# Kernel optimization log

Hardware: AMD Instinct MI355X
Metric: run time of the kernel (lower is better)

The kernel has to match this reference:

```python
import jax, jax.numpy as jnp
import numpy as np

HIDDEN = 512
REL = 16
N = 256
BSZ = 32


def setup_inputs() -> dict:
    key = jax.random.key(0)
    ks = jax.random.split(key, 8)
    columns = jax.random.normal(ks[0], (BSZ, N, HIDDEN), dtype=jnp.float32)
    logits = jax.random.normal(ks[1], (BSZ, N, 2), dtype=jnp.float32)
    adj = jax.random.randint(ks[2], (BSZ, N, N), 0, REL)
    # proj: Linear(2+hidden, hidden); stored as [in, out] so x @ W_proj + b_proj
    W_proj = jax.random.normal(ks[3], (2 + HIDDEN, HIDDEN), dtype=jnp.float32) / np.sqrt(2 + HIDDEN)
    b_proj = jnp.zeros((HIDDEN,), dtype=jnp.float32)
    ln_g = jnp.ones((HIDDEN,), dtype=jnp.float32)
    ln_b = jnp.zeros((HIDDEN,), dtype=jnp.float32)
    # low-rank relation weights: W [h,3,h], V [R,3] (xavier-ish)
    W = jax.random.normal(ks[4], (HIDDEN, 3, HIDDEN), dtype=jnp.float32) * np.sqrt(2.0 / (HIDDEN + HIDDEN))
    V = jax.random.normal(ks[5], (REL, 3), dtype=jnp.float32) * np.sqrt(2.0 / (REL + 3))
    return {"columns": columns, "logits": logits, "adj": adj,
            "W_proj": W_proj, "b_proj": b_proj, "ln_g": ln_g, "ln_b": ln_b,
            "W": W, "V": V}


def reference(columns, logits, adj, W_proj, b_proj, ln_g, ln_b, W, V):
    # proj + layernorm + gelu (dropout is identity in deterministic reference)
    h = jnp.concatenate([columns, logits], axis=-1) @ W_proj + b_proj  # [b,n,h]
    mu = jnp.mean(h, axis=-1, keepdims=True)
    var = jnp.mean(jnp.square(h - mu), axis=-1, keepdims=True)
    h = (h - mu) * jax.lax.rsqrt(var + 1e-5) * ln_g + ln_b
    x = jax.nn.gelu(h, approximate=False)  # torch nn.GELU default = exact erf

    R = V.shape[0]
    # low-rank relation weight mixing: Wr[r] = sum_t V[r,t] * W[:,t,:] -> [R,h,h]
    Wr = jnp.einsum('rt,hto->rho', V, W)

    # relation 0 uses identity adjacency (support = x); relations 1..R-1 use adj==r masks
    masks = (adj[..., None] == jnp.arange(1, R)).astype(x.dtype)  # [b,n,n,R-1]
    sup = jnp.einsum('bnmr,bmh->brnh', masks, x)                  # [b,R-1,n,h]

    out = jnp.einsum('bnh,ho->bno', x, Wr[0]) + jnp.einsum('brnh,rho->bno', sup, Wr[1:])
    return out
```

## Files before the change

### kernel.cpp

```cpp
#include <hip/hip_runtime.h>
#include <math.h>

#define HID 512
#define NSEQ 256
#define BSZ 32
#define ROWS (BSZ*NSEQ)
#define KP 576

typedef _Float16 half8_t __attribute__((ext_vector_type(8)));
typedef _Float16 half4_t __attribute__((ext_vector_type(4)));
typedef float f32x4 __attribute__((ext_vector_type(4)));

__device__ __forceinline__ void gload16(const _Float16* g, _Float16* l) {
    __builtin_amdgcn_global_load_lds(
        (const __attribute__((address_space(1))) unsigned int*)g,
        (__attribute__((address_space(3))) unsigned int*)l, 16, 0, 0);
}

__global__ __launch_bounds__(256) void prep(
    const float* __restrict__ cols, const float* __restrict__ logits,
    const float* __restrict__ Wp, const float* __restrict__ W,
    const int* __restrict__ adj, const float* __restrict__ V,
    _Float16* __restrict__ Acat, _Float16* __restrict__ WpT,
    _Float16* __restrict__ WcT, _Float16* __restrict__ C16b)
{
    __shared__ _Float16 ts[64][68];
    __shared__ _Float16 lutH[48];
    __shared__ _Float16 V0h[3];
    const int blk = blockIdx.x, tid = threadIdx.x;

    if (blk < 1024) {
        int row0 = blk * 8;
        #pragma unroll
        for (int rr = 0; rr < 8; ++rr) {
            int row = row0 + rr;
            for (int k = tid; k < KP; k += 256) {
                float v = 0.f;
                if (k < 512) v = cols[(size_t)row*512 + k];
                else if (k < 514) v = logits[(size_t)row*2 + (k-512)];
                Acat[(size_t)row*KP + k] = (_Float16)v;
            }
        }
    } else if (blk < 1216) {
        int sub = blk - 1024;
        int c0 = (sub % 24) * 64, h0 = (sub / 24) * 64;
        int r = tid >> 2, q = tid & 3;
        #pragma unroll
        for (int i = 0; i < 4; ++i) {
            float4 v = *(const float4*)&W[(size_t)(h0+r)*1536 + c0 + q*16 + i*4];
            ts[r][q*16+i*4+0] = (_Float16)v.x;
            ts[r][q*16+i*4+1] = (_Float16)v.y;
            ts[r][q*16+i*4+2] = (_Float16)v.z;
            ts[r][q*16+i*4+3] = (_Float16)v.w;
        }
        __syncthreads();
        _Float16* op = WcT + (size_t)(c0 + r)*512 + h0 + q*16;
        #pragma unroll
        for (int i = 0; i < 4; ++i) {
            half4_t o;
            #pragma unroll
            for (int j = 0; j < 4; ++j) o[j] = ts[q*16+i*4+j][r];
            *(half4_t*)(op + i*4) = o;
        }
    } else if (blk < 1288) {
        int sub = blk - 1216;
        int k0 = (sub % 9) * 64, o0 = (sub / 9) * 64;
        int r = tid >> 2, q = tid & 3;
        int k = k0 + r;
        #pragma unroll
        for (int i = 0; i < 4; ++i) {
            float4 v = make_float4(0.f,0.f,0.f,0.f);
            if (k < 514) v = *(const float4*)&Wp[(size_t)k*HID + o0 + q*16 + i*4];
            ts[r][q*16+i*4+0] = (_Float16)v.x;
            ts[r][q*16+i*4+1] = (_Float16)v.y;
            ts[r][q*16+i*4+2] = (_Float16)v.z;
            ts[r][q*16+i*4+3] = (_Float16)v.w;
        }
        __syncthreads();
        _Float16* op = WpT + (size_t)(o0 + r)*KP + k0 + q*16;
        #pragma unroll
        for (int i = 0; i < 4; ++i) {
            half4_t o;
            #pragma unroll
            for (int j = 0; j < 4; ++j) o[j] = ts[q*16+i*4+j][r];
            *(half4_t*)(op + i*4) = o;
        }
    } else {
        if (tid < 48) { int r = tid/3; lutH[tid] = (_Float16)((r >= 1) ? V[tid] : 0.f); }
        if (tid < 3) V0h[tid] = (_Float16)V[tid];
        __syncthreads();
        int sub = blk - 1288;
        int b = sub >> 2, nt = sub & 3;
        int w = tid >> 6, lane = tid & 63;
        #pragma unroll
        for (int i = 0; i < 16; ++i) {
            int n = nt*64 + w*16 + i;
            int4 a4 = *(const int4*)(adj + ((size_t)(b*NSEQ + n))*NSEQ + lane*4);
            int av[4] = { a4.x, a4.y, a4.z, a4.w };
            size_t ob = ((size_t)(b*NSEQ + n))*768 + lane*4;
            #pragma unroll
            for (int t = 0; t < 3; ++t) {
                half4_t o;
                #pragma unroll
                for (int j = 0; j < 4; ++j) o[j] = lutH[av[j]*3 + t];
                if ((n >> 2) == lane) o[n & 3] = (_Float16)(o[n & 3] + V0h[t]);
                *(half4_t*)(C16b + ob + (size_t)t*256) = o;
            }
        }
    }
}

template<int KS, int NKT, int DEPTH, int NB, int NBLK, int EPI>
__global__ __launch_bounds__(512) void gemm512(
    const _Float16* __restrict__ A, const _Float16* __restrict__ Bm,
    const float* __restrict__ bias, void* __restrict__ outv)
{
    __shared__ _Float16 smem[DEPTH * 2 * 8192];
    _Float16* As = smem;
    _Float16* Bs = smem + DEPTH * 8192;
    const int tid = threadIdx.x;
    const int w = tid >> 6, lane = tid & 63;
    const int ell = blockIdx.x;
    const int s = (ell & 7) * (NB / 8) + (ell >> 3);
    const int row0 = (s / NBLK) * 128, col0 = (s % NBLK) * 128;
    const int wr = (w >> 2) * 64, wc = (w & 3) * 32;
    const _Float16* Ag = A + (size_t)row0 * KS;
    const _Float16* Bg = (EPI == 2)
        ? Bm + (size_t)(row0 >> 8) * 512 * KS + (size_t)col0 * KS
        : Bm + (size_t)col0 * KS;

    f32x4 acc[4][2] = {};

    auto stage = [&](int kt, int bi) {
        const _Float16* ga = Ag + kt * 64;
        const _Float16* gb = Bg + kt * 64;
        _Float16* la = As + bi * 8192;
        _Float16* lb = Bs + bi * 8192;
        #pragma unroll
        for (int l = 0; l < 2; ++l) {
            int gw = w * 128 + l * 64;
            int g  = gw + lane;
            int row = g >> 3;
            int c   = (g & 7) ^ (row & 7);
            gload16(ga + (size_t)row * KS + c * 8, la + gw * 8);
        }
        #pragma unroll
        for (int l = 0; l < 2; ++l) {
            int gw = w * 128 + l * 64;
            int g  = gw + lane;
            int row = g >> 3;
            int c   = (g & 7) ^ (row & 7);
            gload16(gb + (size_t)row * KS + c * 8, lb + gw * 8);
        }
    };

    auto compute = [&](int bi) {
        const _Float16* Ab = As + bi * 8192;
        const _Float16* Bb = Bs + bi * 8192;
        const int r16 = lane & 15;
        #pragma unroll
        for (int kh = 0; kh < 2; ++kh) {
            const int ks = (lane >> 4) + kh * 4;
            half8_t a[4], b[2];
            #pragma unroll
            for (int mi = 0; mi < 4; ++mi) {
                int row = wr + mi * 16 + r16;
                a[mi] = *(const half8_t*)(Ab + row * 64 + ((ks ^ (row & 7)) * 8));
            }
            #pragma unroll
            for (int ni = 0; ni < 2; ++ni) {
                int col = wc + ni * 16 + r16;
                b[ni] = *(const half8_t*)(Bb + col * 64 + ((ks ^ (col & 7)) * 8));
            }
            #pragma unroll
            for (int mi = 0; mi < 4; ++mi)
                #pragma unroll
                for (int ni = 0; ni < 2; ++ni)
                    acc[mi][ni] = __builtin_amdgcn_mfma_f32_16x16x32_f16(
                        a[mi], b[ni], acc[mi][ni], 0, 0, 0);
        }
    };

    #pragma unroll
    for (int i = 0; i < DEPTH; ++i) stage(i, i);

    int buf = 0;
    #pragma unroll 1
    for (int kt = 0; kt < NKT - (DEPTH - 1); ++kt) {
        if constexpr (DEPTH == 2) asm volatile("s_waitcnt vmcnt(4)" ::: "memory");
        else                      asm volatile("s_waitcnt vmcnt(8)" ::: "memory");
        __builtin_amdgcn_s_barrier();
        __builtin_amdgcn_s_setprio(1);
        compute(buf);
        __builtin_amdgcn_s_setprio(0);
        asm volatile("" ::: "memory");
        __builtin_amdgcn_s_barrier();
        if (kt + DEPTH < NKT) stage(kt + DEPTH, buf);
        ++buf; if (buf == DEPTH) buf = 0;
    }
    if constexpr (DEPTH == 3) {
        asm volatile("s_waitcnt vmcnt(4)" ::: "memory");
        __builtin_amdgcn_s_barrier();
        __builtin_amdgcn_s_setprio(1);
        compute(buf);
        __builtin_amdgcn_s_setprio(0);
        asm volatile("" ::: "memory");
        __builtin_amdgcn_s_barrier();
        ++buf; if (buf == DEPTH) buf = 0;
    }
    asm volatile("s_waitcnt vmcnt(0)" ::: "memory");
    __builtin_amdgcn_s_barrier();
    compute(buf);

    if constexpr (EPI == 2) {
        float* out = (float*)outv;
        #pragma unroll
        for (int mi = 0; mi < 4; ++mi) {
            int r = row0 + wr + mi * 16 + (lane >> 4) * 4;
            #pragma unroll
            for (int ni = 0; ni < 2; ++ni) {
                int cidx = col0 + wc + ni * 16 + (lane & 15);
                #pragma unroll
                for (int q = 0; q < 4; ++q)
                    out[(size_t)(r + q) * HID + cidx] = acc[mi][ni][q];
            }
        }
    } else if constexpr (EPI == 0) {
        __syncthreads();
        _Float16* ep = smem;
        #pragma unroll
        for (int mi = 0; mi < 4; ++mi) {
            int rb = wr + mi * 16 + (lane >> 4) * 4;
            #pragma unroll
            for (int ni = 0; ni < 2; ++ni) {
                int c = wc + ni * 16 + (lane & 15);
                float bv = bias[col0 + c];
                #pragma unroll
                for (int q = 0; q < 4; ++q)
                    ep[(rb + q) * 136 + c] = (_Float16)(acc[mi][ni][q] + bv);
            }
        }
        __syncthreads();
        _Float16* ob = (_Float16*)outv + (size_t)row0 * HID + col0;
        #pragma unroll
        for (int it = 0; it < 4; ++it) {
            int g = it * 512 + tid;
            int r = g >> 4, c8 = g & 15;
            *(half8_t*)(ob + (size_t)r * HID + c8 * 8) =
                *(const half8_t*)&ep[r * 136 + c8 * 8];
        }
    } else {
        __syncthreads();
        _Float16* ep = smem;
        #pragma unroll
        for (int mi = 0; mi < 4; ++mi) {
            int rb = wr + mi * 16 + (lane >> 4) * 4;
            #pragma unroll
            for (int ni = 0; ni < 2; ++ni) {
                int c = wc + ni * 16 + (lane & 15);
                half4_t h4;
                #pragma unroll
                for (int q = 0; q < 4; ++q) h4[q] = (_Float16)acc[mi][ni][q];
                *(half4_t*)&ep[c * 136 + rb] = h4;
            }
        }
        __syncthreads();
        const int b = row0 >> 8, m0 = row0 & 255, t = col0 >> 9, o0 = col0 & 511;
        _Float16* yb = (_Float16*)outv + ((size_t)b * 512 + o0) * 768 + (size_t)t * 256 + m0;
        #pragma unroll
        for (int it = 0; it < 4; ++it) {
            int g = it * 512 + tid;
            int c = g >> 4, m8 = g & 15;
            *(half8_t*)(yb + (size_t)c * 768 + m8 * 8) =
                *(const half8_t*)&ep[c * 136 + m8 * 8];
        }
    }
}

__global__ __launch_bounds__(256) void ln_gelu_ip(_Float16* __restrict__ h,
    const float* __restrict__ g, const float* __restrict__ bb)
{
    int row = blockIdx.x;
    int tid = threadIdx.x;
    float v0 = (float)h[(size_t)row*512 + tid];
    float v1 = (float)h[(size_t)row*512 + 256 + tid];
    __shared__ float red[4];
    int wid = tid >> 6, lane = tid & 63;

    float s = v0 + v1;
    #pragma unroll
    for (int off = 32; off; off >>= 1) s += __shfl_down(s, off);
    if (lane == 0) red[wid] = s;
    __syncthreads();
    float mu = (red[0]+red[1]+red[2]+red[3]) * (1.f/512.f);
    __syncthreads();

    float d0 = v0 - mu, d1 = v1 - mu;
    float q = d0*d0 + d1*d1;
    #pragma unroll
    for (int off = 32; off; off >>= 1) q += __shfl_down(q, off);
    if (lane == 0) red[wid] = q;
    __syncthreads();
    float var = (red[0]+red[1]+red[2]+red[3]) * (1.f/512.f);
    float rs = rsqrtf(var + 1e-5f);

    float y0 = d0*rs*g[tid] + bb[tid];
    float y1 = d1*rs*g[tid+256] + bb[tid+256];
    y0 = 0.5f*y0*(1.f + erff(y0*0.70710678118654752f));
    y1 = 0.5f*y1*(1.f + erff(y1*0.70710678118654752f));
    h[(size_t)row*512 + tid]       = (_Float16)y0;
    h[(size_t)row*512 + 256 + tid] = (_Float16)y1;
}

extern "C" void kernel_launch(void* const* d_in, const int* in_sizes, int n_in,
                              void* d_out, int out_size, void* d_ws, size_t ws_size,
                              hipStream_t stream)
{
    const float* cols   = (const float*)d_in[0];
    const float* logits = (const float*)d_in[1];
    const int*   adj    = (const int*)  d_in[2];
    const float* Wp     = (const float*)d_in[3];
    const float* bp     = (const float*)d_in[4];
    const float* lg     = (const float*)d_in[5];
    const float* lb     = (const float*)d_in[6];
    const float* W      = (const float*)d_in[7];
    const float* V      = (const float*)d_in[8];
    float* out  = (float*)d_out;

    char* p = (char*)d_ws;
    _Float16* Xh   = (_Float16*)p;  p += (size_t)ROWS*HID*2;
    _Float16* Acat = (_Float16*)p;  p += (size_t)ROWS*KP*2;
    _Float16* WpT  = (_Float16*)p;  p += (size_t)HID*KP*2;
    _Float16* WcT  = (_Float16*)p;  p += (size_t)1536*HID*2;
    _Float16* C16b = (_Float16*)p;  p += (size_t)ROWS*768*2;
    _Float16* YTb  = (_Float16*)p;  p += (size_t)BSZ*HID*768*2;

    prep<<<1416, 256, 0, stream>>>(cols, logits, Wp, W, adj, V, Acat, WpT, WcT, C16b);
    gemm512<KP, 9, 3, 256, 4, 0><<<256, 512, 0, stream>>>(Acat, WpT, bp, Xh);
    ln_gelu_ip<<<ROWS, 256, 0, stream>>>(Xh, lg, lb);
    gemm512<512, 8, 2, 768, 12, 1><<<768, 512, 0, stream>>>(Xh, WcT, nullptr, YTb);
    gemm512<768, 12, 3, 256, 4, 2><<<256, 512, 0, stream>>>(C16b, YTb, nullptr, out);
}
```

Measured before the change: 67.87 us.

## Fuse projection GEMM with LayerNorm+GELU and read fp32 inputs directly

Replaces the Acat fp16 staging pass, the projection GEMM and the separate LayerNorm/GELU kernel with one proj_ln kernel. Each block computes full 512-wide rows for 32 rows, converts the fp32 columns and logits to fp16 in registers, reduces row statistics in registers and shared memory, and writes GELU output once. This removes the Acat write and read, the fp16 h round trip and two launches. The cost is a full-width B tile per block (64KB LDS double buffer) with unstaged A loads from global, and variance computed as E[x^2]-mu^2.

```diff
diff --git a/kernel.cpp b/kernel.cpp
--- a/kernel.cpp
+++ b/kernel.cpp
@@ -18,32 +18,18 @@
 }
 
 __global__ __launch_bounds__(256) void prep(
-    const float* __restrict__ cols, const float* __restrict__ logits,
     const float* __restrict__ Wp, const float* __restrict__ W,
     const int* __restrict__ adj, const float* __restrict__ V,
-    _Float16* __restrict__ Acat, _Float16* __restrict__ WpT,
-    _Float16* __restrict__ WcT, _Float16* __restrict__ C16b)
+    _Float16* __restrict__ WpT, _Float16* __restrict__ WcT,
+    _Float16* __restrict__ C16b)
 {
     __shared__ _Float16 ts[64][68];
     __shared__ _Float16 lutH[48];
     __shared__ _Float16 V0h[3];
     const int blk = blockIdx.x, tid = threadIdx.x;
 
-    if (blk < 1024) {
-        int row0 = blk * 8;
-        #pragma unroll
-        for (int rr = 0; rr < 8; ++rr) {
-            int row = row0 + rr;
-            for (int k = tid; k < KP; k += 256) {
-                float v = 0.f;
-                if (k < 512) v = cols[(size_t)row*512 + k];
-                else if (k < 514) v = logits[(size_t)row*2 + (k-512)];
-                Acat[(size_t)row*KP + k] = (_Float16)v;
-            }
-        }
-    } else if (blk < 1216) {
-        int sub = blk - 1024;
-        int c0 = (sub % 24) * 64, h0 = (sub / 24) * 64;
+    if (blk < 192) {
+        int c0 = (blk % 24) * 64, h0 = (blk / 24) * 64;
         int r = tid >> 2, q = tid & 3;
         #pragma unroll
         for (int i = 0; i < 4; ++i) {
@@ -62,8 +48,8 @@
             for (int j = 0; j < 4; ++j) o[j] = ts[q*16+i*4+j][r];
             *(half4_t*)(op + i*4) = o;
         }
-    } else if (blk < 1288) {
-        int sub = blk - 1216;
+    } else if (blk < 264) {
+        int sub = blk - 192;
         int k0 = (sub % 9) * 64, o0 = (sub / 9) * 64;
         int r = tid >> 2, q = tid & 3;
         int k = k0 + r;
@@ -89,7 +75,7 @@
         if (tid < 48) { int r = tid/3; lutH[tid] = (_Float16)((r >= 1) ? V[tid] : 0.f); }
         if (tid < 3) V0h[tid] = (_Float16)V[tid];
         __syncthreads();
-        int sub = blk - 1288;
+        int sub = blk - 264;
         int b = sub >> 2, nt = sub & 3;
         int w = tid >> 6, lane = tid & 63;
         #pragma unroll
@@ -110,10 +96,156 @@
     }
 }
 
+__global__ __launch_bounds__(512) void proj_ln(
+    const float* __restrict__ cols, const float* __restrict__ logits,
+    const _Float16* __restrict__ WpT, const float* __restrict__ bp,
+    const float* __restrict__ lg, const float* __restrict__ lb,
+    _Float16* __restrict__ Xh)
+{
+    __shared__ _Float16 smem[2*32768];
+    __shared__ float redw[8][32][2];
+    __shared__ float redf[32][2];
+    const int tid = threadIdx.x;
+    const int w = tid >> 6, lane = tid & 63;
+    const int r16 = lane & 15, g4 = lane >> 4;
+    const int row0 = blockIdx.x * 32;
+
+    f32x4 acc[2][4] = {};
+
+    auto stage = [&](int kt, int bi) {
+        _Float16* lb_ = smem + bi * 32768;
+        #pragma unroll
+        for (int l = 0; l < 8; ++l) {
+            int gw = w * 512 + l * 64;
+            int g  = gw + lane;
+            int colr = g >> 3;
+            int c    = (g & 7) ^ (colr & 7);
+            gload16(WpT + (size_t)colr * KP + kt * 64 + c * 8, smem + bi*32768 + gw * 8);
+            (void)lb_;
+        }
+    };
+
+    auto compute = [&](int kt, int bi) {
+        const _Float16* Bb = smem + bi * 32768;
+        #pragma unroll
+        for (int kh = 0; kh < 2; ++kh) {
+            const int ks = g4 + kh * 4;
+            const int k  = kt * 64 + ks * 8;
+            half8_t a[2], b[4];
+            #pragma unroll
+            for (int mi = 0; mi < 2; ++mi) {
+                int row = row0 + mi * 16 + r16;
+                if (kt < 8) {
+                    float4 f0 = *(const float4*)&cols[(size_t)row * 512 + k];
+                    float4 f1 = *(const float4*)&cols[(size_t)row * 512 + k + 4];
+                    a[mi][0]=(_Float16)f0.x; a[mi][1]=(_Float16)f0.y;
+                    a[mi][2]=(_Float16)f0.z; a[mi][3]=(_Float16)f0.w;
+                    a[mi][4]=(_Float16)f1.x; a[mi][5]=(_Float16)f1.y;
+                    a[mi][6]=(_Float16)f1.z; a[mi][7]=(_Float16)f1.w;
+                } else {
+                    float l0 = 0.f, l1 = 0.f;
+                    if (ks == 0) { l0 = logits[(size_t)row*2]; l1 = logits[(size_t)row*2+1]; }
+                    a[mi][0]=(_Float16)l0; a[mi][1]=(_Float16)l1;
+                    a[mi][2]=0; a[mi][3]=0; a[mi][4]=0; a[mi][5]=0; a[mi][6]=0; a[mi][7]=0;
+                }
+            }
+            #pragma unroll
+            for (int ni = 0; ni < 4; ++ni) {
+                int col = w * 64 + ni * 16 + r16;
+                b[ni] = *(const half8_t*)(Bb + col * 64 + ((ks ^ (col & 7)) * 8));
+            }
+            #pragma unroll
+            for (int mi = 0; mi < 2; ++mi)
+                #pragma unroll
+                for (int ni = 0; ni < 4; ++ni)
+                    acc[mi][ni] = __builtin_amdgcn_mfma_f32_16x16x32_f16(
+                        a[mi], b[ni], acc[mi][ni], 0, 0, 0);
+        }
+    };
+
+    stage(0, 0);
+    int buf = 0;
+    #pragma unroll 1
+    for (int kt = 0; kt < 9; ++kt) {
+        __syncthreads();
+        if (kt < 8) stage(kt + 1, buf ^ 1);
+        compute(kt, buf);
+        buf ^= 1;
+    }
+    __syncthreads();
+
+    #pragma unroll
+    for (int ni = 0; ni < 4; ++ni) {
+        float bv = bp[w * 64 + ni * 16 + r16];
+        #pragma unroll
+        for (int mi = 0; mi < 2; ++mi)
+            #pragma unroll
+            for (int q = 0; q < 4; ++q) acc[mi][ni][q] += bv;
+    }
+    #pragma unroll
+    for (int mi = 0; mi < 2; ++mi) {
+        #pragma unroll
+        for (int q = 0; q < 4; ++q) {
+            float s = 0.f, s2 = 0.f;
+            #pragma unroll
+            for (int ni = 0; ni < 4; ++ni) {
+                float v = acc[mi][ni][q];
+                s += v; s2 += v * v;
+            }
+            #pragma unroll
+            for (int msk = 1; msk < 16; msk <<= 1) {
+                s  += __shfl_xor(s,  msk);
+                s2 += __shfl_xor(s2, msk);
+            }
+            if (r16 == 0) {
+                int row = mi * 16 + g4 * 4 + q;
+                redw[w][row][0] = s;
+                redw[w][row][1] = s2;
+            }
+        }
+    }
+    __syncthreads();
+    if (tid < 64) {
+        int row = tid >> 1, j = tid & 1;
+        float v = 0.f;
+        #pragma unroll
+        for (int ww = 0; ww < 8; ++ww) v += redw[ww][row][j];
+        redf[row][j] = v;
+    }
+    __syncthreads();
+
+    _Float16* ep = smem;
+    #pragma unroll
+    for (int mi = 0; mi < 2; ++mi) {
+        #pragma unroll
+        for (int q = 0; q < 4; ++q) {
+            int row = mi * 16 + g4 * 4 + q;
+            float mu = redf[row][0] * (1.f/512.f);
+            float var = redf[row][1] * (1.f/512.f) - mu * mu;
+            float rs = rsqrtf(var + 1e-5f);
+            #pragma unroll
+            for (int ni = 0; ni < 4; ++ni) {
+                int col = w * 64 + ni * 16 + r16;
+                float y = (acc[mi][ni][q] - mu) * rs * lg[col] + lb[col];
+                y = 0.5f * y * (1.f + erff(y * 0.70710678118654752f));
+                ep[row * 520 + col] = (_Float16)y;
+            }
+        }
+    }
+    __syncthreads();
+    #pragma unroll
+    for (int it = 0; it < 4; ++it) {
+        int g = it * 512 + tid;
+        int row = g >> 6, c8 = g & 63;
+        *(half8_t*)(Xh + (size_t)(row0 + row) * 512 + c8 * 8) =
+            *(const half8_t*)&ep[row * 520 + c8 * 8];
+    }
+}
+
 template<int KS, int NKT, int DEPTH, int NB, int NBLK, int EPI>
 __global__ __launch_bounds__(512) void gemm512(
     const _Float16* __restrict__ A, const _Float16* __restrict__ Bm,
-    const float* __restrict__ bias, void* __restrict__ outv)
+    void* __restrict__ outv)
 {
     __shared__ _Float16 smem[DEPTH * 2 * 8192];
     _Float16* As = smem;
@@ -225,30 +357,6 @@
                     out[(size_t)(r + q) * HID + cidx] = acc[mi][ni][q];
             }
         }
-    } else if constexpr (EPI == 0) {
-        __syncthreads();
-        _Float16* ep = smem;
-        #pragma unroll
-        for (int mi = 0; mi < 4; ++mi) {
-            int rb = wr + mi * 16 + (lane >> 4) * 4;
-            #pragma unroll
-            for (int ni = 0; ni < 2; ++ni) {
-                int c = wc + ni * 16 + (lane & 15);
-                float bv = bias[col0 + c];
-                #pragma unroll
-                for (int q = 0; q < 4; ++q)
-                    ep[(rb + q) * 136 + c] = (_Float16)(acc[mi][ni][q] + bv);
-            }
-        }
-        __syncthreads();
-        _Float16* ob = (_Float16*)outv + (size_t)row0 * HID + col0;
-        #pragma unroll
-        for (int it = 0; it < 4; ++it) {
-            int g = it * 512 + tid;
-            int r = g >> 4, c8 = g & 15;
-            *(half8_t*)(ob + (size_t)r * HID + c8 * 8) =
-                *(const half8_t*)&ep[r * 136 + c8 * 8];
-        }
     } else {
         __syncthreads();
         _Float16* ep = smem;
@@ -275,41 +383,6 @@
                 *(const half8_t*)&ep[c * 136 + m8 * 8];
         }
     }
-}
-
-__global__ __launch_bounds__(256) void ln_gelu_ip(_Float16* __restrict__ h,
-    const float* __restrict__ g, const float* __restrict__ bb)
-{
-    int row = blockIdx.x;
-    int tid = threadIdx.x;
-    float v0 = (float)h[(size_t)row*512 + tid];
-    float v1 = (float)h[(size_t)row*512 + 256 + tid];
-    __shared__ float red[4];
-    int wid = tid >> 6, lane = tid & 63;
-
-    float s = v0 + v1;
-    #pragma unroll
-    for (int off = 32; off; off >>= 1) s += __shfl_down(s, off);
-    if (lane == 0) red[wid] = s;
-    __syncthreads();
-    float mu = (red[0]+red[1]+red[2]+red[3]) * (1.f/512.f);
-    __syncthreads();
-
-    float d0 = v0 - mu, d1 = v1 - mu;
-    float q = d0*d0 + d1*d1;
-    #pragma unroll
-    for (int off = 32; off; off >>= 1) q += __shfl_down(q, off);
-    if (lane == 0) red[wid] = q;
-    __syncthreads();
-    float var = (red[0]+red[1]+red[2]+red[3]) * (1.f/512.f);
-    float rs = rsqrtf(var + 1e-5f);
-
-    float y0 = d0*rs*g[tid] + bb[tid];
-    float y1 = d1*rs*g[tid+256] + bb[tid+256];
-    y0 = 0.5f*y0*(1.f + erff(y0*0.70710678118654752f));
-    y1 = 0.5f*y1*(1.f + erff(y1*0.70710678118654752f));
-    h[(size_t)row*512 + tid]       = (_Float16)y0;
-    h[(size_t)row*512 + 256 + tid] = (_Float16)y1;
 }
 
 extern "C" void kernel_launch(void* const* d_in, const int* in_sizes, int n_in,
@@ -329,15 +402,13 @@
 
     char* p = (char*)d_ws;
     _Float16* Xh   = (_Float16*)p;  p += (size_t)ROWS*HID*2;
-    _Float16* Acat = (_Float16*)p;  p += (size_t)ROWS*KP*2;
     _Float16* WpT  = (_Float16*)p;  p += (size_t)HID*KP*2;
     _Float16* WcT  = (_Float16*)p;  p += (size_t)1536*HID*2;
     _Float16* C16b = (_Float16*)p;  p += (size_t)ROWS*768*2;
     _Float16* YTb  = (_Float16*)p;  p += (size_t)BSZ*HID*768*2;
 
-    prep<<<1416, 256, 0, stream>>>(cols, logits, Wp, W, adj, V, Acat, WpT, WcT, C16b);
-    gemm512<KP, 9, 3, 256, 4, 0><<<256, 512, 0, stream>>>(Acat, WpT, bp, Xh);
-    ln_gelu_ip<<<ROWS, 256, 0, stream>>>(Xh, lg, lb);
-    gemm512<512, 8, 2, 768, 12, 1><<<768, 512, 0, stream>>>(Xh, WcT, nullptr, YTb);
-    gemm512<768, 12, 3, 256, 4, 2><<<256, 512, 0, stream>>>(C16b, YTb, nullptr, out);
+    prep<<<392, 256, 0, stream>>>(Wp, W, adj, V, WpT, WcT, C16b);
+    proj_ln<<<256, 512, 0, stream>>>(cols, logits, WpT, bp, lg, lb, Xh);
+    gemm512<512, 8, 2, 768, 12, 1><<<768, 512, 0, stream>>>(Xh, WcT, YTb);
+    gemm512<768, 12, 3, 256, 4, 2><<<256, 512, 0, stream>>>(C16b, YTb, out);
 }
```

New measurement: 77.33 us. 1.14x slower.

## Replace final aggregation GEMM with dedicated 256x64 tile kernel

Applied to the files above, without the earlier changes.

The last batched GEMM (C16b times per-batch YTb) moves from the generic 128x128 tile kernel to a dedicated kernel. Each block now covers a full 256-row batch slice and 64 output columns, with 8 waves arranged 4x2 and a 3-stage LDS pipeline. The per-batch A slice is loaded once per column tile, with the aim of better reuse and scheduling for the batch-indexed B operand. The block count stays at 256, but each block's tile shape and LDS footprint differ, which changes occupancy and load balance.

```diff
diff --git a/kernel.cpp b/kernel.cpp
--- a/kernel.cpp
+++ b/kernel.cpp
@@ -125,9 +125,7 @@
     const int row0 = (s / NBLK) * 128, col0 = (s % NBLK) * 128;
     const int wr = (w >> 2) * 64, wc = (w & 3) * 32;
     const _Float16* Ag = A + (size_t)row0 * KS;
-    const _Float16* Bg = (EPI == 2)
-        ? Bm + (size_t)(row0 >> 8) * 512 * KS + (size_t)col0 * KS
-        : Bm + (size_t)col0 * KS;
+    const _Float16* Bg = Bm + (size_t)col0 * KS;
 
     f32x4 acc[4][2] = {};
 
@@ -212,20 +210,7 @@
     __builtin_amdgcn_s_barrier();
     compute(buf);
 
-    if constexpr (EPI == 2) {
-        float* out = (float*)outv;
-        #pragma unroll
-        for (int mi = 0; mi < 4; ++mi) {
-            int r = row0 + wr + mi * 16 + (lane >> 4) * 4;
-            #pragma unroll
-            for (int ni = 0; ni < 2; ++ni) {
-                int cidx = col0 + wc + ni * 16 + (lane & 15);
-                #pragma unroll
-                for (int q = 0; q < 4; ++q)
-                    out[(size_t)(r + q) * HID + cidx] = acc[mi][ni][q];
-            }
-        }
-    } else if constexpr (EPI == 0) {
+    if constexpr (EPI == 0) {
         __syncthreads();
         _Float16* ep = smem;
         #pragma unroll
@@ -273,6 +258,112 @@
             int c = g >> 4, m8 = g & 15;
             *(half8_t*)(yb + (size_t)c * 768 + m8 * 8) =
                 *(const half8_t*)&ep[c * 136 + m8 * 8];
+        }
+    }
+}
+
+__global__ __launch_bounds__(512) void aggout(
+    const _Float16* __restrict__ C16b, const _Float16* __restrict__ YTb,
+    float* __restrict__ out)
+{
+    __shared__ _Float16 smem[61440];
+    _Float16* As = smem;
+    _Float16* Bs = smem + 49152;
+    const int tid = threadIdx.x;
+    const int w = tid >> 6, lane = tid & 63;
+    const int ell = blockIdx.x;
+    const int s = (ell & 7) * 32 + (ell >> 3);
+    const int b = s >> 3, col0 = (s & 7) * 64;
+    const int wr = (w >> 1) * 64, wc = (w & 1) * 32;
+    const _Float16* Ag = C16b + (size_t)b * NSEQ * 768;
+    const _Float16* Bg = YTb + ((size_t)b * 512 + col0) * 768;
+
+    f32x4 acc[4][2] = {};
+
+    auto stage = [&](int kt, int bi) {
+        const _Float16* ga = Ag + kt * 64;
+        const _Float16* gb = Bg + kt * 64;
+        _Float16* la = As + bi * 16384;
+        _Float16* lb = Bs + bi * 4096;
+        #pragma unroll
+        for (int l = 0; l < 4; ++l) {
+            int gw = w * 256 + l * 64;
+            int g  = gw + lane;
+            int row = g >> 3;
+            int c   = (g & 7) ^ (row & 7);
+            gload16(ga + (size_t)row * 768 + c * 8, la + gw * 8);
+        }
+        {
+            int gw = w * 64;
+            int g  = gw + lane;
+            int row = g >> 3;
+            int c   = (g & 7) ^ (row & 7);
+            gload16(gb + (size_t)row * 768 + c * 8, lb + gw * 8);
+        }
+    };
+
+    auto compute = [&](int bi) {
+        const _Float16* Ab = As + bi * 16384;
+        const _Float16* Bb = Bs + bi * 4096;
+        const int r16 = lane & 15;
+        #pragma unroll
+        for (int kh = 0; kh < 2; ++kh) {
+            const int ks = (lane >> 4) + kh * 4;
+            half8_t a[4], bfr[2];
+            #pragma unroll
+            for (int mi = 0; mi < 4; ++mi) {
+                int row = wr + mi * 16 + r16;
+                a[mi] = *(const half8_t*)(Ab + row * 64 + ((ks ^ (row & 7)) * 8));
+            }
+            #pragma unroll
+            for (int ni = 0; ni < 2; ++ni) {
+                int col = wc + ni * 16 + r16;
+                bfr[ni] = *(const half8_t*)(Bb + col * 64 + ((ks ^ (col & 7)) * 8));
+            }
+            #pragma unroll
+            for (int mi = 0; mi < 4; ++mi)
+                #pragma unroll
+                for (int ni = 0; ni < 2; ++ni)
+                    acc[mi][ni] = __builtin_amdgcn_mfma_f32_16x16x32_f16(
+                        a[mi], bfr[ni], acc[mi][ni], 0, 0, 0);
+        }
+    };
+
+    stage(0, 0); stage(1, 1); stage(2, 2);
+    int buf = 0;
+    #pragma unroll 1
+    for (int kt = 0; kt < 10; ++kt) {
+        asm volatile("s_waitcnt vmcnt(10)" ::: "memory");
+        __builtin_amdgcn_s_barrier();
+        __builtin_amdgcn_s_setprio(1);
+        compute(buf);
+        __builtin_amdgcn_s_setprio(0);
+        asm volatile("" ::: "memory");
+        __builtin_amdgcn_s_barrier();
+        if (kt + 3 < 12) stage(kt + 3, buf);
+        ++buf; if (buf == 3) buf = 0;
+    }
+    asm volatile("s_waitcnt vmcnt(5)" ::: "memory");
+    __builtin_amdgcn_s_barrier();
+    __builtin_amdgcn_s_setprio(1);
+    compute(buf);
+    __builtin_amdgcn_s_setprio(0);
+    asm volatile("" ::: "memory");
+    __builtin_amdgcn_s_barrier();
+    ++buf; if (buf == 3) buf = 0;
+    asm volatile("s_waitcnt vmcnt(0)" ::: "memory");
+    __builtin_amdgcn_s_barrier();
+    compute(buf);
+
+    #pragma unroll
+    for (int mi = 0; mi < 4; ++mi) {
+        int r = b * NSEQ + wr + mi * 16 + (lane >> 4) * 4;
+        #pragma unroll
+        for (int ni = 0; ni < 2; ++ni) {
+            int cidx = col0 + wc + ni * 16 + (lane & 15);
+            #pragma unroll
+            for (int q = 0; q < 4; ++q)
+                out[(size_t)(r + q) * HID + cidx] = acc[mi][ni][q];
         }
     }
 }
@@ -339,5 +430,5 @@
     gemm512<KP, 9, 3, 256, 4, 0><<<256, 512, 0, stream>>>(Acat, WpT, bp, Xh);
     ln_gelu_ip<<<ROWS, 256, 0, stream>>>(Xh, lg, lb);
     gemm512<512, 8, 2, 768, 12, 1><<<768, 512, 0, stream>>>(Xh, WcT, nullptr, YTb);
-    gemm512<768, 12, 3, 256, 4, 2><<<256, 512, 0, stream>>>(C16b, YTb, nullptr, out);
-}
+    aggout<<<256, 512, 0, stream>>>(C16b, YTb, out);
+}
```

Measured after the change: 68.58 us. About the same (+1.1%).

## Fuse fp32-to-fp16 activation conversion into projection GEMM loading fp32 directly

Applied to the files above, without the earlier changes.

Removes the prep stage that converted columns/logits into a padded fp16 Acat buffer. A new projection GEMM loads fp32 columns straight into LDS, converts to fp16 in registers before MFMA, and handles the two logit columns as a separate final K step from a small LDS tile. The aim is to drop the Acat write and reread traffic. In exchange it uses a smaller 64x128 tile with 512 blocks and does extra conversion work inside the inner loop.

```diff
diff --git a/kernel.cpp b/kernel.cpp
--- a/kernel.cpp
+++ b/kernel.cpp
@@ -10,40 +10,32 @@
 typedef _Float16 half8_t __attribute__((ext_vector_type(8)));
 typedef _Float16 half4_t __attribute__((ext_vector_type(4)));
 typedef float f32x4 __attribute__((ext_vector_type(4)));
+typedef float f32x8 __attribute__((ext_vector_type(8)));
 
 __device__ __forceinline__ void gload16(const _Float16* g, _Float16* l) {
     __builtin_amdgcn_global_load_lds(
         (const __attribute__((address_space(1))) unsigned int*)g,
         (__attribute__((address_space(3))) unsigned int*)l, 16, 0, 0);
 }
+__device__ __forceinline__ void gload16f(const float* g, float* l) {
+    __builtin_amdgcn_global_load_lds(
+        (const __attribute__((address_space(1))) unsigned int*)g,
+        (__attribute__((address_space(3))) unsigned int*)l, 16, 0, 0);
+}
 
 __global__ __launch_bounds__(256) void prep(
-    const float* __restrict__ cols, const float* __restrict__ logits,
     const float* __restrict__ Wp, const float* __restrict__ W,
     const int* __restrict__ adj, const float* __restrict__ V,
-    _Float16* __restrict__ Acat, _Float16* __restrict__ WpT,
-    _Float16* __restrict__ WcT, _Float16* __restrict__ C16b)
+    _Float16* __restrict__ WpT, _Float16* __restrict__ WcT,
+    _Float16* __restrict__ C16b)
 {
     __shared__ _Float16 ts[64][68];
     __shared__ _Float16 lutH[48];
     __shared__ _Float16 V0h[3];
     const int blk = blockIdx.x, tid = threadIdx.x;
 
-    if (blk < 1024) {
-        int row0 = blk * 8;
-        #pragma unroll
-        for (int rr = 0; rr < 8; ++rr) {
-            int row = row0 + rr;
-            for (int k = tid; k < KP; k += 256) {
-                float v = 0.f;
-                if (k < 512) v = cols[(size_t)row*512 + k];
-                else if (k < 514) v = logits[(size_t)row*2 + (k-512)];
-                Acat[(size_t)row*KP + k] = (_Float16)v;
-            }
-        }
-    } else if (blk < 1216) {
-        int sub = blk - 1024;
-        int c0 = (sub % 24) * 64, h0 = (sub / 24) * 64;
+    if (blk < 192) {
+        int c0 = (blk % 24) * 64, h0 = (blk / 24) * 64;
         int r = tid >> 2, q = tid & 3;
         #pragma unroll
         for (int i = 0; i < 4; ++i) {
@@ -62,8 +54,8 @@
             for (int j = 0; j < 4; ++j) o[j] = ts[q*16+i*4+j][r];
             *(half4_t*)(op + i*4) = o;
         }
-    } else if (blk < 1288) {
-        int sub = blk - 1216;
+    } else if (blk < 264) {
+        int sub = blk - 192;
         int k0 = (sub % 9) * 64, o0 = (sub / 9) * 64;
         int r = tid >> 2, q = tid & 3;
         int k = k0 + r;
@@ -89,7 +81,7 @@
         if (tid < 48) { int r = tid/3; lutH[tid] = (_Float16)((r >= 1) ? V[tid] : 0.f); }
         if (tid < 3) V0h[tid] = (_Float16)V[tid];
         __syncthreads();
-        int sub = blk - 1288;
+        int sub = blk - 264;
         int b = sub >> 2, nt = sub & 3;
         int w = tid >> 6, lane = tid & 63;
         #pragma unroll
@@ -110,10 +102,163 @@
     }
 }
 
+__global__ __launch_bounds__(512) void projx(
+    const float* __restrict__ cols, const float* __restrict__ logits,
+    const _Float16* __restrict__ WpT, const float* __restrict__ bp,
+    _Float16* __restrict__ Xh)
+{
+    __shared__ float    Asf[2*4096];
+    __shared__ _Float16 Bsm[2*8192];
+    __shared__ _Float16 Lt[4096];
+    const int tid = threadIdx.x;
+    const int w = tid >> 6, lane = tid & 63;
+    const int r16 = lane & 15, g4 = lane >> 4;
+    const int ell = blockIdx.x;
+    const int s = (ell & 7) * 64 + (ell >> 3);
+    const int row0 = (s >> 2) * 64, col0 = (s & 3) * 128;
+    const int wr = (w >> 2) * 32, wc = (w & 3) * 32;
+
+    f32x4 acc[2][2] = {};
+
+    *(half8_t*)(Lt + tid * 8) = half8_t{0,0,0,0,0,0,0,0};
+    if (tid < 64) {
+        int row = tid;
+        float2 lv = *(const float2*)&logits[(size_t)(row0 + row) * 2];
+        Lt[row * 64 + (row & 7) * 8 + 0] = (_Float16)lv.x;
+        Lt[row * 64 + (row & 7) * 8 + 1] = (_Float16)lv.y;
+    }
+
+    auto stage = [&](int kt, int bi, bool doA) {
+        if (doA) {
+            #pragma unroll
+            for (int l = 0; l < 2; ++l) {
+                int gw = w * 128 + l * 64;
+                int g  = gw + lane;
+                int row = g >> 4, cg = g & 15;
+                int c = (((cg >> 1) ^ (row & 7)) << 1) | (cg & 1);
+                gload16f(cols + (size_t)(row0 + row) * 512 + kt * 64 + c * 4,
+                         Asf + bi * 4096 + gw * 4);
+            }
+        }
+        #pragma unroll
+        for (int l = 0; l < 2; ++l) {
+            int gw = w * 128 + l * 64;
+            int g  = gw + lane;
+            int colr = g >> 3;
+            int c    = (g & 7) ^ (colr & 7);
+            gload16(WpT + (size_t)(col0 + colr) * KP + kt * 64 + c * 8,
+                    Bsm + bi * 8192 + gw * 8);
+        }
+    };
+
+    auto computeF = [&](int bi) {
+        const float*    Ab = Asf + bi * 4096;
+        const _Float16* Bb = Bsm + bi * 8192;
+        #pragma unroll
+        for (int kh = 0; kh < 2; ++kh) {
+            const int ks = g4 + kh * 4;
+            half8_t a[2], b[2];
+            #pragma unroll
+            for (int mi = 0; mi < 2; ++mi) {
+                int row = wr + mi * 16 + r16;
+                f32x8 af = *(const f32x8*)(Ab + row * 64 + ((ks ^ (row & 7)) * 8));
+                #pragma unroll
+                for (int j = 0; j < 8; ++j) a[mi][j] = (_Float16)af[j];
+            }
+            #pragma unroll
+            for (int ni = 0; ni < 2; ++ni) {
+                int col = wc + ni * 16 + r16;
+                b[ni] = *(const half8_t*)(Bb + col * 64 + ((ks ^ (col & 7)) * 8));
+            }
+            #pragma unroll
+            for (int mi = 0; mi < 2; ++mi)
+                #pragma unroll
+                for (int ni = 0; ni < 2; ++ni)
+                    acc[mi][ni] = __builtin_amdgcn_mfma_f32_16x16x32_f16(
+                        a[mi], b[ni], acc[mi][ni], 0, 0, 0);
+        }
+    };
+
+    auto computeL = [&](int bi) {
+        const _Float16* Bb = Bsm + bi * 8192;
+        #pragma unroll
+        for (int kh = 0; kh < 2; ++kh) {
+            const int ks = g4 + kh * 4;
+            half8_t a[2], b[2];
+            #pragma unroll
+            for (int mi = 0; mi < 2; ++mi) {
+                int row = wr + mi * 16 + r16;
+                a[mi] = *(const half8_t*)(Lt + row * 64 + ((ks ^ (row & 7)) * 8));
+            }
+            #pragma unroll
+            for (int ni = 0; ni < 2; ++ni) {
+                int col = wc + ni * 16 + r16;
+                b[ni] = *(const half8_t*)(Bb + col * 64 + ((ks ^ (col & 7)) * 8));
+            }
+            #pragma unroll
+            for (int mi = 0; mi < 2; ++mi)
+                #pragma unroll
+                for (int ni = 0; ni < 2; ++ni)
+                    acc[mi][ni] = __builtin_amdgcn_mfma_f32_16x16x32_f16(
+                        a[mi], b[ni], acc[mi][ni], 0, 0, 0);
+        }
+    };
+
+    stage(0, 0, true);
+    stage(1, 1, true);
+    int buf = 0;
+    #pragma unroll 1
+    for (int kt = 0; kt < 7; ++kt) {
+        asm volatile("s_waitcnt vmcnt(4)" ::: "memory");
+        __builtin_amdgcn_s_barrier();
+        __builtin_amdgcn_s_setprio(1);
+        computeF(buf);
+        __builtin_amdgcn_s_setprio(0);
+        asm volatile("" ::: "memory");
+        __builtin_amdgcn_s_barrier();
+        stage(kt + 2, buf, kt + 2 < 8);
+        buf ^= 1;
+    }
+    asm volatile("s_waitcnt vmcnt(2)" ::: "memory");
+    __builtin_amdgcn_s_barrier();
+    __builtin_amdgcn_s_setprio(1);
+    computeF(buf);
+    __builtin_amdgcn_s_setprio(0);
+    asm volatile("" ::: "memory");
+    __builtin_amdgcn_s_barrier();
+    buf ^= 1;
+    asm volatile("s_waitcnt vmcnt(0)" ::: "memory");
+    __builtin_amdgcn_s_barrier();
+    computeL(buf);
+
+    __syncthreads();
+    _Float16* ep = (_Float16*)Asf;
+    #pragma unroll
+    for (int mi = 0; mi < 2; ++mi) {
+        int rb = wr + mi * 16 + g4 * 4;
+        #pragma unroll
+        for (int ni = 0; ni < 2; ++ni) {
+            int c = wc + ni * 16 + r16;
+            float bv = bp[col0 + c];
+            #pragma unroll
+            for (int q = 0; q < 4; ++q)
+                ep[(rb + q) * 136 + c] = (_Float16)(acc[mi][ni][q] + bv);
+        }
+    }
+    __syncthreads();
+    #pragma unroll
+    for (int it = 0; it < 2; ++it) {
+        int g = it * 512 + tid;
+        int row = g >> 4, c8 = g & 15;
+        *(half8_t*)(Xh + (size_t)(row0 + row) * 512 + col0 + c8 * 8) =
+            *(const half8_t*)&ep[row * 136 + c8 * 8];
+    }
+}
+
 template<int KS, int NKT, int DEPTH, int NB, int NBLK, int EPI>
 __global__ __launch_bounds__(512) void gemm512(
     const _Float16* __restrict__ A, const _Float16* __restrict__ Bm,
-    const float* __restrict__ bias, void* __restrict__ outv)
+    void* __restrict__ outv)
 {
     __shared__ _Float16 smem[DEPTH * 2 * 8192];
     _Float16* As = smem;
@@ -225,30 +370,6 @@
                     out[(size_t)(r + q) * HID + cidx] = acc[mi][ni][q];
             }
         }
-    } else if constexpr (EPI == 0) {
-        __syncthreads();
-        _Float16* ep = smem;
-        #pragma unroll
-        for (int mi = 0; mi < 4; ++mi) {
-            int rb = wr + mi * 16 + (lane >> 4) * 4;
-            #pragma unroll
-            for (int ni = 0; ni < 2; ++ni) {
-                int c = wc + ni * 16 + (lane & 15);
-                float bv = bias[col0 + c];
-                #pragma unroll
-                for (int q = 0; q < 4; ++q)
-                    ep[(rb + q) * 136 + c] = (_Float16)(acc[mi][ni][q] + bv);
-            }
-        }
-        __syncthreads();
-        _Float16* ob = (_Float16*)outv + (size_t)row0 * HID + col0;
-        #pragma unroll
-        for (int it = 0; it < 4; ++it) {
-            int g = it * 512 + tid;
-            int r = g >> 4, c8 = g & 15;
-            *(half8_t*)(ob + (size_t)r * HID + c8 * 8) =
-                *(const half8_t*)&ep[r * 136 + c8 * 8];
-        }
     } else {
         __syncthreads();
         _Float16* ep = smem;
@@ -329,15 +450,14 @@
 
     char* p = (char*)d_ws;
     _Float16* Xh   = (_Float16*)p;  p += (size_t)ROWS*HID*2;
-    _Float16* Acat = (_Float16*)p;  p += (size_t)ROWS*KP*2;
     _Float16* WpT  = (_Float16*)p;  p += (size_t)HID*KP*2;
     _Float16* WcT  = (_Float16*)p;  p += (size_t)1536*HID*2;
     _Float16* C16b = (_Float16*)p;  p += (size_t)ROWS*768*2;
     _Float16* YTb  = (_Float16*)p;  p += (size_t)BSZ*HID*768*2;
 
-    prep<<<1416, 256, 0, stream>>>(cols, logits, Wp, W, adj, V, Acat, WpT, WcT, C16b);
-    gemm512<KP, 9, 3, 256, 4, 0><<<256, 512, 0, stream>>>(Acat, WpT, bp, Xh);
+    prep<<<392, 256, 0, stream>>>(Wp, W, adj, V, WpT, WcT, C16b);
+    projx<<<512, 512, 0, stream>>>(cols, logits, WpT, bp, Xh);
     ln_gelu_ip<<<ROWS, 256, 0, stream>>>(Xh, lg, lb);
-    gemm512<512, 8, 2, 768, 12, 1><<<768, 512, 0, stream>>>(Xh, WcT, nullptr, YTb);
-    gemm512<768, 12, 3, 256, 4, 2><<<256, 512, 0, stream>>>(C16b, YTb, nullptr, out);
-}
+    gemm512<512, 8, 2, 768, 12, 1><<<768, 512, 0, stream>>>(Xh, WcT, YTb);
+    gemm512<768, 12, 3, 256, 4, 2><<<256, 512, 0, stream>>>(C16b, YTb, out);
+}
```

Measured after the change: 64.90 us. -4.4%, faster.
